# Kernel optimization log

Measured on AMD Instinct MI355X. Metric: run time of the kernel, lower is better.

Reference implementation:

```python
import jax, jax.numpy as jnp
import numpy as np

EPS = 1e-6
NH = 8     # num_head
WIN = 7    # window

def _ln(x, w, b):
    # channels_last LayerNorm over the final dim
    m = x.mean(-1, keepdims=True)
    v = ((x - m) ** 2).mean(-1, keepdims=True)
    return (x - m) / jnp.sqrt(v + EPS) * w + b

def _dwconv7(x, w, b):
    # x: (B, C, H, W); w: (C, 1, 7, 7) depthwise kernel; padding 3 (SAME for k=7)
    y = jax.lax.conv_general_dilated(
        x, w, window_strides=(1, 1), padding=((3, 3), (3, 3)),
        feature_group_count=x.shape[1],
        dimension_numbers=('NCHW', 'OIHW', 'NCHW'))
    return y + b[None, :, None, None]

def _forward(x, x_e, ln_w, ln_b, lne_w, lne_b, q_w, q_b, qcut_w, qcut_b,
             a_w, a_b, l_w, l_b, conv_w, conv_b, econv_w, econv_b,
             efore_w, efore_b, eback_w, eback_b, kv_w, kv_b,
             scl_w, scl_b, proj_w, proj_b, proje_w, proje_b):
    B, H, W, C = x.shape
    hd = C // NH // 2  # attention head dim (kv is split into k and v halves)

    xn = _ln(x, ln_w, ln_b)          # (B,H,W,C)
    xen = _ln(x_e, lne_w, lne_b)     # (B,H,W,C//2)

    # global shortcut branch (window != 0)
    short = jnp.concatenate([xn, xen], axis=3).transpose(0, 3, 1, 2)  # (B, 3C/2, H, W)

    q = xn @ q_w + q_b                # (B,H,W,C)
    cut = xn @ qcut_w + qcut_b        # (B,H,W,C//2)

    xl = jax.nn.gelu(xn @ l_w + l_b, approximate=False).transpose(0, 3, 1, 2)  # (B,C,H,W)
    a = _dwconv7(xl, conv_w, conv_b).transpose(0, 2, 3, 1) @ a_w + a_b          # (B,H,W,C)

    # kv from the activated l-branch (pre-conv)
    bfeat = xl.transpose(0, 2, 3, 1)                                  # (B,H,W,C)
    kv = (bfeat @ kv_w + kv_b).reshape(B, H * W, 2, NH, hd).transpose(2, 0, 3, 1, 4)
    k, v = kv[0], kv[1]                                               # (B,NH,HW,hd)

    # AdaptiveAvgPool2d((7,7)); H,W divisible by 7 -> exact uniform block mean
    pooled = short.reshape(B, -1, WIN, H // WIN, WIN, W // WIN).mean(axis=(3, 5))  # (B,3C/2,7,7)
    pooled = pooled.transpose(0, 2, 3, 1) @ scl_w + scl_b             # (B,7,7,C//2)
    m = pooled.reshape(B, WIN * WIN, NH, hd).transpose(0, 2, 1, 3)    # (B,NH,49,hd)

    attn = jax.nn.softmax((m * hd ** -0.5) @ jnp.swapaxes(k, -2, -1), axis=-1)  # (B,NH,49,HW)
    ao = (attn @ v).reshape(B, NH, WIN, WIN, hd).transpose(0, 1, 4, 2, 3).reshape(B, C // 2, WIN, WIN)
    ao = jax.image.resize(ao, (B, C // 2, H, W), method='bilinear').transpose(0, 2, 3, 1)  # (B,H,W,C//2)

    # depth branch: linear -> depthwise conv -> linear
    xe2 = (xen @ efore_w + efore_b).transpose(0, 3, 1, 2)             # (B,C//2,H,W)
    xe2 = _dwconv7(xe2, econv_w, econv_b).transpose(0, 2, 3, 1) @ eback_w + eback_b

    cut = cut * xe2
    xg = q * a
    cat = jnp.concatenate([xg, ao, cut], axis=3)                      # (B,H,W,2C)
    x_e_out = cat @ proje_w + proje_b                                 # (B,H,W,C//2)
    x_out = cat @ proj_w + proj_b                                     # (B,H,W,C)
    return x_out, x_e_out

def setup_inputs() -> dict:
    B, H, W, C = 16, 56, 84, 256
    key = jax.random.key(0)
    ks = jax.random.split(key, 16)
    def lin(k, din, dout):
        return jax.random.normal(k, (din, dout), jnp.float32) * float(1.0 / np.sqrt(din))
    return {
        'x': jax.random.normal(ks[0], (B, H, W, C), jnp.float32),
        'x_e': jax.random.normal(ks[1], (B, H, W, C // 2), jnp.float32),
        'ln_w': jnp.ones((C,), jnp.float32), 'ln_b': jnp.zeros((C,), jnp.float32),
        'lne_w': jnp.ones((C // 2,), jnp.float32), 'lne_b': jnp.zeros((C // 2,), jnp.float32),
        'q_w': lin(ks[2], C, C), 'q_b': jnp.zeros((C,), jnp.float32),
        'qcut_w': lin(ks[3], C, C // 2), 'qcut_b': jnp.zeros((C // 2,), jnp.float32),
        'a_w': lin(ks[4], C, C), 'a_b': jnp.zeros((C,), jnp.float32),
        'l_w': lin(ks[5], C, C), 'l_b': jnp.zeros((C,), jnp.float32),
        'conv_w': jax.random.normal(ks[6], (C, 1, 7, 7), jnp.float32) * 0.05,
        'conv_b': jnp.zeros((C,), jnp.float32),
        'econv_w': jax.random.normal(ks[7], (C // 2, 1, 7, 7), jnp.float32) * 0.05,
        'econv_b': jnp.zeros((C // 2,), jnp.float32),
        'efore_w': lin(ks[8], C // 2, C // 2), 'efore_b': jnp.zeros((C // 2,), jnp.float32),
        'eback_w': lin(ks[9], C // 2, C // 2), 'eback_b': jnp.zeros((C // 2,), jnp.float32),
        'kv_w': lin(ks[10], C, C), 'kv_b': jnp.zeros((C,), jnp.float32),
        'scl_w': lin(ks[11], C // 2 * 3, C // 2), 'scl_b': jnp.zeros((C // 2,), jnp.float32),
        'proj_w': lin(ks[12], 2 * C, C), 'proj_b': jnp.zeros((C,), jnp.float32),
        'proje_w': lin(ks[13], 2 * C, C // 2), 'proje_b': jnp.zeros((C // 2,), jnp.float32),
    }

def reference(x, x_e, ln_w, ln_b, lne_w, lne_b, q_w, q_b, qcut_w, qcut_b,
              a_w, a_b, l_w, l_b, conv_w, conv_b, econv_w, econv_b,
              efore_w, efore_b, eback_w, eback_b, kv_w, kv_b,
              scl_w, scl_b, proj_w, proj_b, proje_w, proje_b):
    return _forward(x, x_e, ln_w, ln_b, lne_w, lne_b, q_w, q_b, qcut_w, qcut_b,
                    a_w, a_b, l_w, l_b, conv_w, conv_b, econv_w, econv_b,
                    efore_w, efore_b, eback_w, eback_b, kv_w, kv_b,
                    scl_w, scl_b, proj_w, proj_b, proje_w, proje_b)
```

## Files before the change

### kernel.cpp

```cpp
#include <hip/hip_runtime.h>
#include <math.h>

#define N_TOK 75264
#define BDIM 16
#define HDIM 56
#define WDIM 84
#define CDIM 256
#define NHEAD 8
#define HWTOK 4704
#define NQ 49
#define SPLIT 8
#define TOKSPL 588
#define TSUB 84

typedef unsigned short u16;
typedef __attribute__((ext_vector_type(8))) short short8;
typedef __attribute__((ext_vector_type(8))) unsigned short ushort8;
typedef __attribute__((ext_vector_type(4))) float floatx4;

__device__ __forceinline__ float bf2f(u16 u) {
    return __builtin_bit_cast(float, (unsigned)u << 16);
}
__device__ __forceinline__ u16 f2bf(float f) {
    unsigned u = __builtin_bit_cast(unsigned, f);
    u += 0x7fffu + ((u >> 16) & 1u);
    return (u16)(u >> 16);
}
__device__ __forceinline__ float gelu_exact(float v) {
    return 0.5f * v * (1.0f + erff(v * 0.70710678118654752f));
}

__global__ __launch_bounds__(256)
void wsplit_kernel(const float* __restrict__ q, const float* __restrict__ qcut,
                   const float* __restrict__ a, const float* __restrict__ l,
                   const float* __restrict__ kv, const float* __restrict__ efo,
                   const float* __restrict__ eba, const float* __restrict__ proj,
                   const float* __restrict__ proje,
                   u16* __restrict__ dh, u16* __restrict__ dl)
{
    int e = blockIdx.x * 256 + threadIdx.x;
    const float* src; int N, base, le;
    if (e < 65536)       { src = q;     N = 256; base = 0;      le = e; }
    else if (e < 98304)  { src = qcut;  N = 128; base = 65536;  le = e - 65536; }
    else if (e < 163840) { src = a;     N = 256; base = 98304;  le = e - 98304; }
    else if (e < 229376) { src = l;     N = 256; base = 163840; le = e - 163840; }
    else if (e < 294912) { src = kv;    N = 256; base = 229376; le = e - 229376; }
    else if (e < 311296) { src = efo;   N = 128; base = 294912; le = e - 294912; }
    else if (e < 327680) { src = eba;   N = 128; base = 311296; le = e - 311296; }
    else if (e < 458752) { src = proj;  N = 256; base = 327680; le = e - 327680; }
    else                 { src = proje; N = 128; base = 458752; le = e - 458752; }
    int K = (base >= 327680) ? 512 : ((base >= 294912) ? 128 : 256);
    int k = le / N, n = le & (N - 1);
    float w = src[le];
    u16 h = f2bf(w);
    dh[base + n * K + k] = h;
    dl[base + n * K + k] = f2bf(w - bf2f(h));
}

__global__ __launch_bounds__(256)
void cwt_kernel(const float* __restrict__ conv_w, const float* __restrict__ econv_w,
                float* __restrict__ wt)
{
    int i = blockIdx.x * 256 + threadIdx.x;
    if (i < 12544) {
        int c = i / 49, tap = i % 49;
        wt[tap * 256 + c] = conv_w[i];
    } else if (i < 18816) {
        int j = i - 12544;
        int c = j / 49, tap = j % 49;
        wt[12544 + tap * 128 + c] = econv_w[j];
    }
}

template<int CH>
__global__ __launch_bounds__(256)
void ln_kernel(const float* __restrict__ x, const float* __restrict__ w,
               const float* __restrict__ b, u16* __restrict__ oh, u16* __restrict__ ol)
{
    const int lane = threadIdx.x & 63;
    const int wv = threadIdx.x >> 6;
    const size_t tok = (size_t)blockIdx.x * 4 + wv;
    constexpr int V = CH / 64;
    float v[V];
    float s = 0.f, sq = 0.f;
    if constexpr (CH == 256) {
        float4 t4 = *(const float4*)(x + tok * CH + lane * 4);
        v[0] = t4.x; v[1] = t4.y; v[2] = t4.z; v[3] = t4.w;
    } else {
        float2 t2 = *(const float2*)(x + tok * CH + lane * 2);
        v[0] = t2.x; v[1] = t2.y;
    }
    #pragma unroll
    for (int i = 0; i < V; ++i) { s += v[i]; sq += v[i] * v[i]; }
    #pragma unroll
    for (int off = 32; off > 0; off >>= 1) {
        s += __shfl_xor(s, off);
        sq += __shfl_xor(sq, off);
    }
    const float mean = s * (1.0f / CH);
    const float var = sq * (1.0f / CH) - mean * mean;
    const float rstd = rsqrtf(var + 1e-6f);
    u16 hh[V], ll[V];
    #pragma unroll
    for (int i = 0; i < V; ++i) {
        float o = (v[i] - mean) * rstd * w[lane * V + i] + b[lane * V + i];
        hh[i] = f2bf(o);
        ll[i] = f2bf(o - bf2f(hh[i]));
    }
    if constexpr (CH == 256) {
        ushort4 th = {hh[0], hh[1], hh[2], hh[3]};
        ushort4 tl = {ll[0], ll[1], ll[2], ll[3]};
        *(ushort4*)(oh + tok * CH + lane * 4) = th;
        *(ushort4*)(ol + tok * CH + lane * 4) = tl;
    } else {
        ushort2 th = {hh[0], hh[1]};
        ushort2 tl = {ll[0], ll[1]};
        *(ushort2*)(oh + tok * CH + lane * 2) = th;
        *(ushort2*)(ol + tok * CH + lane * 2) = tl;
    }
}

__global__ __launch_bounds__(128)
void pool_scl_kernel(const u16* __restrict__ xnh, const u16* __restrict__ xnl,
                     const u16* __restrict__ xeh, const u16* __restrict__ xel,
                     const float* __restrict__ sclw, const float* __restrict__ sclb,
                     float* __restrict__ m)
{
    __shared__ float pooled[384];
    const int bp = blockIdx.x;
    const int b = bp / 49, p = bp % 49;
    const int py = p / 7, px = p % 7;
    const int tid = threadIdx.x;
    for (int ch = tid; ch < 384; ch += 128) {
        float acc = 0.f;
        for (int i = 0; i < 96; ++i) {
            int y = py * 8 + i / 12, x = px * 12 + i % 12;
            size_t pix = ((size_t)(b * HDIM + y) * WDIM + x);
            if (ch < 256) acc += bf2f(xnh[pix * 256 + ch]) + bf2f(xnl[pix * 256 + ch]);
            else          acc += bf2f(xeh[pix * 128 + ch - 256]) + bf2f(xel[pix * 128 + ch - 256]);
        }
        pooled[ch] = acc * (1.0f / 96.0f);
    }
    __syncthreads();
    float acc = sclb[tid];
    for (int k = 0; k < 384; ++k) acc = fmaf(pooled[k], sclw[k * 128 + tid], acc);
    m[(size_t)bp * 128 + tid] = acc;
}

#define BK 32
#define PADK 40
template<int EPI>
__global__ __launch_bounds__(256, 2)
void mgemm(const u16* __restrict__ Ah, const u16* __restrict__ Al, int lda,
           const u16* __restrict__ Bh, const u16* __restrict__ Bl, int K,
           const float* __restrict__ bias,
           u16* __restrict__ Dh, u16* __restrict__ Dl,
           float* __restrict__ Df, int ldd)
{
    __shared__ u16 AsH[128 * PADK], AsL[128 * PADK], BsH[128 * PADK], BsL[128 * PADK];
    const int t = threadIdx.x;
    const int m0 = blockIdx.x * 128, n0 = blockIdx.y * 128;
    const int sr = t >> 1;
    const int sk = (t & 1) * 16;
    const int lane = t & 63;
    const int w = t >> 6;
    const int wm = w >> 1, wn = w & 1;
    const int frow = lane & 15;
    const int fko = (lane >> 4) * 8;

    const u16* pAh = Ah + (size_t)(m0 + sr) * lda + sk;
    const u16* pAl = Al + (size_t)(m0 + sr) * lda + sk;
    const u16* pBh = Bh + (size_t)(n0 + sr) * K + sk;
    const u16* pBl = Bl + (size_t)(n0 + sr) * K + sk;

    int4 rAh0 = *(const int4*)(pAh);     int4 rAh1 = *(const int4*)(pAh + 8);
    int4 rAl0 = *(const int4*)(pAl);     int4 rAl1 = *(const int4*)(pAl + 8);
    int4 rBh0 = *(const int4*)(pBh);     int4 rBh1 = *(const int4*)(pBh + 8);
    int4 rBl0 = *(const int4*)(pBl);     int4 rBl1 = *(const int4*)(pBl + 8);

    floatx4 acc[4][4] = {};

    for (int k0 = 0; k0 < K; k0 += BK) {
        __syncthreads();
        *(int4*)&AsH[sr * PADK + sk] = rAh0;  *(int4*)&AsH[sr * PADK + sk + 8] = rAh1;
        *(int4*)&AsL[sr * PADK + sk] = rAl0;  *(int4*)&AsL[sr * PADK + sk + 8] = rAl1;
        *(int4*)&BsH[sr * PADK + sk] = rBh0;  *(int4*)&BsH[sr * PADK + sk + 8] = rBh1;
        *(int4*)&BsL[sr * PADK + sk] = rBl0;  *(int4*)&BsL[sr * PADK + sk + 8] = rBl1;
        __syncthreads();
        if (k0 + BK < K) {
            rAh0 = *(const int4*)(pAh + k0 + BK);  rAh1 = *(const int4*)(pAh + k0 + BK + 8);
            rAl0 = *(const int4*)(pAl + k0 + BK);  rAl1 = *(const int4*)(pAl + k0 + BK + 8);
            rBh0 = *(const int4*)(pBh + k0 + BK);  rBh1 = *(const int4*)(pBh + k0 + BK + 8);
            rBl0 = *(const int4*)(pBl + k0 + BK);  rBl1 = *(const int4*)(pBl + k0 + BK + 8);
        }
        short8 afh[4], afl[4], bfh[4], bfl[4];
        #pragma unroll
        for (int i = 0; i < 4; ++i) {
            int ar = wm * 64 + i * 16 + frow;
            afh[i] = *(const short8*)&AsH[ar * PADK + fko];
            afl[i] = *(const short8*)&AsL[ar * PADK + fko];
            int bc = wn * 64 + i * 16 + frow;
            bfh[i] = *(const short8*)&BsH[bc * PADK + fko];
            bfl[i] = *(const short8*)&BsL[bc * PADK + fko];
        }
        #pragma unroll
        for (int mt = 0; mt < 4; ++mt)
        #pragma unroll
        for (int nt = 0; nt < 4; ++nt) {
            acc[mt][nt] = __builtin_amdgcn_mfma_f32_16x16x32_bf16(afh[mt], bfh[nt], acc[mt][nt], 0, 0, 0);
            acc[mt][nt] = __builtin_amdgcn_mfma_f32_16x16x32_bf16(afh[mt], bfl[nt], acc[mt][nt], 0, 0, 0);
            acc[mt][nt] = __builtin_amdgcn_mfma_f32_16x16x32_bf16(afl[mt], bfh[nt], acc[mt][nt], 0, 0, 0);
        }
    }

    #pragma unroll
    for (int mt = 0; mt < 4; ++mt)
    #pragma unroll
    for (int nt = 0; nt < 4; ++nt)
    #pragma unroll
    for (int i = 0; i < 4; ++i) {
        int r = m0 + wm * 64 + mt * 16 + (lane >> 4) * 4 + i;
        int c = n0 + wn * 64 + nt * 16 + (lane & 15);
        float v = acc[mt][nt][i] + bias[c];
        size_t off = (size_t)r * ldd + c;
        if constexpr (EPI == 1) v = gelu_exact(v);
        if constexpr (EPI == 2) v *= bf2f(Dh[off]) + bf2f(Dl[off]);
        if constexpr (EPI == 3) {
            Df[off] = v;
        } else {
            u16 h = f2bf(v);
            Dh[off] = h;
            Dl[off] = f2bf(v - bf2f(h));
        }
    }
}

template<int C>
__global__ __launch_bounds__(256)
void dwconv7_kernel(const u16* __restrict__ inh, const u16* __restrict__ inl,
                    const float* __restrict__ wT, const float* __restrict__ bias,
                    u16* __restrict__ outh, u16* __restrict__ outl)
{
    constexpr int CPW = C / 8;
    const int gid = blockIdx.x * 256 + threadIdx.x;
    const int cw = gid & (CPW - 1);
    const int p = gid / CPW;
    const int c = cw * 8;
    const int x = p % WDIM;
    int tmp = p / WDIM;
    const int y = tmp % HDIM;
    const int b = tmp / HDIM;
    float acc[8];
    {
        float4 b0 = *(const float4*)(bias + c);
        float4 b1 = *(const float4*)(bias + c + 4);
        acc[0] = b0.x; acc[1] = b0.y; acc[2] = b0.z; acc[3] = b0.w;
        acc[4] = b1.x; acc[5] = b1.y; acc[6] = b1.z; acc[7] = b1.w;
    }
    for (int ky = 0; ky < 7; ++ky) {
        int yy = y + ky - 3;
        if (yy < 0 || yy >= HDIM) continue;
        const size_t rowoff = ((size_t)(b * HDIM + yy) * WDIM) * C;
        #pragma unroll
        for (int kx = 0; kx < 7; ++kx) {
            int xx = x + kx - 3;
            if (xx < 0 || xx >= WDIM) continue;
            ushort8 ih = *(const ushort8*)(inh + rowoff + (size_t)xx * C + c);
            ushort8 il = *(const ushort8*)(inl + rowoff + (size_t)xx * C + c);
            const float* wp = wT + (ky * 7 + kx) * C + c;
            float4 w0 = *(const float4*)(wp);
            float4 w1 = *(const float4*)(wp + 4);
            acc[0] = fmaf(bf2f(ih[0]) + bf2f(il[0]), w0.x, acc[0]);
            acc[1] = fmaf(bf2f(ih[1]) + bf2f(il[1]), w0.y, acc[1]);
            acc[2] = fmaf(bf2f(ih[2]) + bf2f(il[2]), w0.z, acc[2]);
            acc[3] = fmaf(bf2f(ih[3]) + bf2f(il[3]), w0.w, acc[3]);
            acc[4] = fmaf(bf2f(ih[4]) + bf2f(il[4]), w1.x, acc[4]);
            acc[5] = fmaf(bf2f(ih[5]) + bf2f(il[5]), w1.y, acc[5]);
            acc[6] = fmaf(bf2f(ih[6]) + bf2f(il[6]), w1.z, acc[6]);
            acc[7] = fmaf(bf2f(ih[7]) + bf2f(il[7]), w1.w, acc[7]);
        }
    }
    ushort8 oh, ol;
    #pragma unroll
    for (int j = 0; j < 8; ++j) {
        u16 h = f2bf(acc[j]);
        oh[j] = h;
        ol[j] = f2bf(acc[j] - bf2f(h));
    }
    *(ushort8*)(outh + (size_t)p * C + c) = oh;
    *(ushort8*)(outl + (size_t)p * C + c) = ol;
}

__global__ __launch_bounds__(256)
void attn_part_kernel(const float* __restrict__ m, const u16* __restrict__ kvh,
                      const u16* __restrict__ kvl,
                      float* __restrict__ Opart, float* __restrict__ mpart,
                      float* __restrict__ lpart)
{
    __shared__ float mq[NQ * 17];
    __shared__ float Ks[TSUB * 16];
    __shared__ float Vs[TSUB * 16];
    __shared__ float St[NQ * 85];
    __shared__ float Osm[NQ * 16];
    __shared__ float rowm[NQ], rowl[NQ], rowscale[NQ], rownewm[NQ];
    const int blk = blockIdx.x;
    const int bh = blk >> 3, s = blk & 7;
    const int b = bh >> 3, h = bh & 7;
    const int tid = threadIdx.x;
    const int tbase = s * TOKSPL;
    for (int i = tid; i < NQ * 16; i += 256) {
        int p = i >> 4, d = i & 15;
        mq[p * 17 + d] = m[((size_t)(b * 49 + p)) * 128 + h * 16 + d] * 0.25f;
        Osm[i] = 0.f;
    }
    if (tid < NQ) { rowm[tid] = -3.4e38f; rowl[tid] = 0.f; }
    __syncthreads();
    for (int c0 = 0; c0 < TOKSPL; c0 += TSUB) {
        const int t0 = tbase + c0;
        for (int i = tid; i < TSUB * 4; i += 256) {
            int row = i >> 2, q = (i & 3) << 2;
            size_t base = ((size_t)(b * HWTOK + t0 + row)) * 256 + h * 16 + q;
            ushort4 kh = *(const ushort4*)(kvh + base);
            ushort4 kl = *(const ushort4*)(kvl + base);
            ushort4 vh = *(const ushort4*)(kvh + base + 128);
            ushort4 vl = *(const ushort4*)(kvl + base + 128);
            Ks[row * 16 + q + 0] = bf2f(kh.x) + bf2f(kl.x);
            Ks[row * 16 + q + 1] = bf2f(kh.y) + bf2f(kl.y);
            Ks[row * 16 + q + 2] = bf2f(kh.z) + bf2f(kl.z);
            Ks[row * 16 + q + 3] = bf2f(kh.w) + bf2f(kl.w);
            Vs[row * 16 + q + 0] = bf2f(vh.x) + bf2f(vl.x);
            Vs[row * 16 + q + 1] = bf2f(vh.y) + bf2f(vl.y);
            Vs[row * 16 + q + 2] = bf2f(vh.z) + bf2f(vl.z);
            Vs[row * 16 + q + 3] = bf2f(vh.w) + bf2f(vl.w);
        }
        __syncthreads();
        for (int i = tid; i < NQ * TSUB; i += 256) {
            int p = i % NQ, t = i / NQ;
            const float* mp = &mq[p * 17];
            const float* kp = &Ks[t * 16];
            float sv = 0.f;
            #pragma unroll
            for (int d = 0; d < 16; ++d) sv = fmaf(mp[d], kp[d], sv);
            St[p * 85 + t] = sv;
        }
        __syncthreads();
        if (tid < NQ) {
            float mx = -3.4e38f;
            const float* sr = &St[tid * 85];
            for (int t = 0; t < TSUB; ++t) mx = fmaxf(mx, sr[t]);
            float nm = fmaxf(rowm[tid], mx);
            rownewm[tid] = nm;
            rowscale[tid] = expf(rowm[tid] - nm);
        }
        __syncthreads();
        for (int i = tid; i < NQ * TSUB; i += 256) {
            int p = i / TSUB, t = i % TSUB;
            St[p * 85 + t] = expf(St[p * 85 + t] - rownewm[p]);
        }
        __syncthreads();
        if (tid < NQ) {
            float sv = 0.f;
            const float* sr = &St[tid * 85];
            for (int t = 0; t < TSUB; ++t) sv += sr[t];
            rowl[tid] = rowl[tid] * rowscale[tid] + sv;
            rowm[tid] = rownewm[tid];
        }
        for (int i = tid; i < NQ * 16; i += 256) {
            int p = i >> 4, d = i & 15;
            float acc = Osm[i] * rowscale[p];
            const float* sr = &St[p * 85];
            const float* vp = &Vs[d];
            #pragma unroll 6
            for (int t = 0; t < TSUB; ++t) acc = fmaf(sr[t], vp[t * 16], acc);
            Osm[i] = acc;
        }
        __syncthreads();
    }
    for (int i = tid; i < NQ * 16; i += 256)
        Opart[(size_t)blk * (NQ * 16) + i] = Osm[i];
    if (tid < NQ) {
        mpart[blk * NQ + tid] = rowm[tid];
        lpart[blk * NQ + tid] = rowl[tid];
    }
}

__global__ __launch_bounds__(256)
void attn_combine_kernel(const float* __restrict__ Opart, const float* __restrict__ mpart,
                         const float* __restrict__ lpart, float* __restrict__ ao)
{
    const int bh = blockIdx.x;
    const int b = bh >> 3, h = bh & 7;
    const int tid = threadIdx.x;
    for (int i = tid; i < NQ * 16; i += 256) {
        int p = i >> 4, d = i & 15;
        float M = -3.4e38f;
        #pragma unroll
        for (int s = 0; s < SPLIT; ++s)
            M = fmaxf(M, mpart[(bh * SPLIT + s) * NQ + p]);
        float sO = 0.f, sl = 0.f;
        #pragma unroll
        for (int s = 0; s < SPLIT; ++s) {
            float e = expf(mpart[(bh * SPLIT + s) * NQ + p] - M);
            sl = fmaf(lpart[(bh * SPLIT + s) * NQ + p], e, sl);
            sO = fmaf(Opart[(size_t)(bh * SPLIT + s) * (NQ * 16) + i], e, sO);
        }
        ao[((size_t)(b * 49 + p)) * 128 + h * 16 + d] = sO / sl;
    }
}

__global__ __launch_bounds__(256)
void resize_kernel(const float* __restrict__ ao, u16* __restrict__ cath,
                   u16* __restrict__ catl)
{
    const int idx = blockIdx.x * 256 + threadIdx.x;
    const int c = idx & 127;
    const int p = idx >> 7;
    const int x = p % WDIM;
    int tmp = p / WDIM;
    const int y = tmp % HDIM;
    const int b = tmp / HDIM;
    float fy = (y + 0.5f) * 0.125f - 0.5f;
    float fx = (x + 0.5f) * (1.0f / 12.0f) - 0.5f;
    float yf = floorf(fy), xf = floorf(fx);
    int y0 = (int)yf, x0 = (int)xf;
    float wy = fy - yf, wx = fx - xf;
    int y1 = y0 + 1 < 6 ? y0 + 1 : 6;
    int x1 = x0 + 1 < 6 ? x0 + 1 : 6;
    y0 = y0 > 0 ? y0 : 0;
    x0 = x0 > 0 ? x0 : 0;
    const float* base = ao + (size_t)b * 49 * 128 + c;
    float v00 = base[(y0 * 7 + x0) * 128], v01 = base[(y0 * 7 + x1) * 128];
    float v10 = base[(y1 * 7 + x0) * 128], v11 = base[(y1 * 7 + x1) * 128];
    float r = (1.f - wy) * ((1.f - wx) * v00 + wx * v01)
            + wy * ((1.f - wx) * v10 + wx * v11);
    u16 h = f2bf(r);
    cath[(size_t)p * 512 + 256 + c] = h;
    catl[(size_t)p * 512 + 256 + c] = f2bf(r - bf2f(h));
}

extern "C" void kernel_launch(void* const* d_in, const int* in_sizes, int n_in,
                              void* d_out, int out_size, void* d_ws, size_t ws_size,
                              hipStream_t stream) {
    const float* x       = (const float*)d_in[0];
    const float* x_e     = (const float*)d_in[1];
    const float* ln_w    = (const float*)d_in[2];
    const float* ln_b    = (const float*)d_in[3];
    const float* lne_w   = (const float*)d_in[4];
    const float* lne_b   = (const float*)d_in[5];
    const float* q_w     = (const float*)d_in[6];
    const float* q_b     = (const float*)d_in[7];
    const float* qcut_w  = (const float*)d_in[8];
    const float* qcut_b  = (const float*)d_in[9];
    const float* a_w     = (const float*)d_in[10];
    const float* a_b     = (const float*)d_in[11];
    const float* l_w     = (const float*)d_in[12];
    const float* l_b     = (const float*)d_in[13];
    const float* conv_w  = (const float*)d_in[14];
    const float* conv_b  = (const float*)d_in[15];
    const float* econv_w = (const float*)d_in[16];
    const float* econv_b = (const float*)d_in[17];
    const float* efore_w = (const float*)d_in[18];
    const float* efore_b = (const float*)d_in[19];
    const float* eback_w = (const float*)d_in[20];
    const float* eback_b = (const float*)d_in[21];
    const float* kv_w    = (const float*)d_in[22];
    const float* kv_b    = (const float*)d_in[23];
    const float* scl_w   = (const float*)d_in[24];
    const float* scl_b   = (const float*)d_in[25];
    const float* proj_w  = (const float*)d_in[26];
    const float* proj_b  = (const float*)d_in[27];
    const float* proje_w = (const float*)d_in[28];
    const float* proje_b = (const float*)d_in[29];

    float* out_x = (float*)d_out;
    float* out_e = out_x + (size_t)N_TOK * 256;

    const size_t NT = N_TOK;

    u16* doutU = (u16*)d_out;
    u16* xlH  = doutU;
    u16* xlL  = xlH  + NT * 256;
    u16* xenH = xlL  + NT * 256;
    u16* xenL = xenH + NT * 128;

    u16* ws   = (u16*)d_ws;
    u16* xnH  = ws;
    u16* xnL  = xnH  + NT * 256;
    u16* catH = xnL  + NT * 256;
    u16* catL = catH + NT * 512;
    u16* wtH  = catL + NT * 512;
    u16* wtL  = wtH  + 524288;
    float* mbuf  = (float*)(wtL + 524288);
    float* aosm  = mbuf + 16 * 49 * 128;
    float* Opart = aosm + 16 * 49 * 128;
    float* mpart = Opart + 1024 * NQ * 16;
    float* lpart = mpart + 1024 * NQ;
    float* cwT   = lpart + 1024 * NQ;
    float* ecwT  = cwT + 12544;

    u16 *qtH = wtH + 0,      *qtL = wtL + 0;
    u16 *qctH = wtH + 65536, *qctL = wtL + 65536;
    u16 *atH = wtH + 98304,  *atL = wtL + 98304;
    u16 *ltH = wtH + 163840, *ltL = wtL + 163840;
    u16 *kvtH = wtH + 229376,*kvtL = wtL + 229376;
    u16 *efH = wtH + 294912, *efL = wtL + 294912;
    u16 *ebH = wtH + 311296, *ebL = wtL + 311296;
    u16 *pjH = wtH + 327680, *pjL = wtL + 327680;
    u16 *peH = wtH + 458752, *peL = wtL + 458752;

    u16 *cvH = xnH, *cvL = xnL;
    u16 *kvH = xnH, *kvL = xnL;
    u16 *e1H = xlH, *e1L = xlH + NT * 128;
    u16 *e2H = xlL, *e2L = xlL + NT * 128;

    dim3 g2(588, 2), g1(588, 1);

    wsplit_kernel<<<2048, 256, 0, stream>>>(q_w, qcut_w, a_w, l_w, kv_w, efore_w,
                                            eback_w, proj_w, proje_w, wtH, wtL);
    cwt_kernel<<<74, 256, 0, stream>>>(conv_w, econv_w, cwT);

    ln_kernel<256><<<N_TOK / 4, 256, 0, stream>>>(x, ln_w, ln_b, xnH, xnL);
    ln_kernel<128><<<N_TOK / 4, 256, 0, stream>>>(x_e, lne_w, lne_b, xenH, xenL);
    pool_scl_kernel<<<16 * 49, 128, 0, stream>>>(xnH, xnL, xenH, xenL, scl_w, scl_b, mbuf);

    mgemm<0><<<g2, 256, 0, stream>>>(xnH, xnL, 256, qtH, qtL, 256, q_b,
                                     catH, catL, nullptr, 512);
    mgemm<0><<<g1, 256, 0, stream>>>(xnH, xnL, 256, qctH, qctL, 256, qcut_b,
                                     catH + 384, catL + 384, nullptr, 512);
    mgemm<1><<<g2, 256, 0, stream>>>(xnH, xnL, 256, ltH, ltL, 256, l_b,
                                     xlH, xlL, nullptr, 256);
    dwconv7_kernel<256><<<(N_TOK * 32) / 256, 256, 0, stream>>>(xlH, xlL, cwT, conv_b, cvH, cvL);
    mgemm<2><<<g2, 256, 0, stream>>>(cvH, cvL, 256, atH, atL, 256, a_b,
                                     catH, catL, nullptr, 512);
    mgemm<0><<<g2, 256, 0, stream>>>(xlH, xlL, 256, kvtH, kvtL, 256, kv_b,
                                     kvH, kvL, nullptr, 256);
    attn_part_kernel<<<BDIM * NHEAD * SPLIT, 256, 0, stream>>>(mbuf, kvH, kvL,
                                                               Opart, mpart, lpart);
    attn_combine_kernel<<<BDIM * NHEAD, 256, 0, stream>>>(Opart, mpart, lpart, aosm);
    resize_kernel<<<(N_TOK * 128) / 256, 256, 0, stream>>>(aosm, catH, catL);

    mgemm<0><<<g1, 256, 0, stream>>>(xenH, xenL, 128, efH, efL, 128, efore_b,
                                     e1H, e1L, nullptr, 128);
    dwconv7_kernel<128><<<(N_TOK * 16) / 256, 256, 0, stream>>>(e1H, e1L, ecwT, econv_b, e2H, e2L);
    mgemm<2><<<g1, 256, 0, stream>>>(e2H, e2L, 128, ebH, ebL, 128, eback_b,
                                     catH + 384, catL + 384, nullptr, 512);
    mgemm<3><<<g2, 256, 0, stream>>>(catH, catL, 512, pjH, pjL, 512, proj_b,
                                     nullptr, nullptr, out_x, 256);
    mgemm<3><<<g1, 256, 0, stream>>>(catH, catL, 512, peH, peL, 512, proje_b,
                                     nullptr, nullptr, out_e, 128);
}
```

Baseline: 1.358 ms.

## Store conv inputs as fp32 and compute four output rows per dwconv thread

The l-branch GELU output and the efore output are now written as fp32 instead of bf16 hi/lo pairs. The kv GEMM gains an A-source mode that reads fp32 and splits it into hi/lo in registers. The depthwise 7x7 conv now computes four vertically adjacent output pixels per thread, so each loaded input row feeds up to four accumulators, and it reads one fp32 buffer instead of two bf16 planes. This is meant to cut global loads in the conv and drop the per-element hi/lo recombination, at the cost of more registers per conv thread and an extra conversion in the kv GEMM load path.

```diff
diff --git a/kernel.cpp b/kernel.cpp
--- a/kernel.cpp
+++ b/kernel.cpp
@@ -149,9 +149,10 @@
 
 #define BK 32
 #define PADK 40
-template<int EPI>
+template<int EPI, int ASRC>
 __global__ __launch_bounds__(256, 2)
-void mgemm(const u16* __restrict__ Ah, const u16* __restrict__ Al, int lda,
+void mgemm(const u16* __restrict__ Ah, const u16* __restrict__ Al,
+           const float* __restrict__ Af, int lda,
            const u16* __restrict__ Bh, const u16* __restrict__ Bl, int K,
            const float* __restrict__ bias,
            u16* __restrict__ Dh, u16* __restrict__ Dl,
@@ -168,30 +169,63 @@
     const int frow = lane & 15;
     const int fko = (lane >> 4) * 8;
 
-    const u16* pAh = Ah + (size_t)(m0 + sr) * lda + sk;
-    const u16* pAl = Al + (size_t)(m0 + sr) * lda + sk;
     const u16* pBh = Bh + (size_t)(n0 + sr) * K + sk;
     const u16* pBl = Bl + (size_t)(n0 + sr) * K + sk;
-
-    int4 rAh0 = *(const int4*)(pAh);     int4 rAh1 = *(const int4*)(pAh + 8);
-    int4 rAl0 = *(const int4*)(pAl);     int4 rAl1 = *(const int4*)(pAl + 8);
     int4 rBh0 = *(const int4*)(pBh);     int4 rBh1 = *(const int4*)(pBh + 8);
     int4 rBl0 = *(const int4*)(pBl);     int4 rBl1 = *(const int4*)(pBl + 8);
 
+    const u16* pAh = nullptr; const u16* pAl = nullptr; const float* pAf = nullptr;
+    int4 rAh0, rAh1, rAl0, rAl1;
+    float4 rf0, rf1, rf2, rf3;
+    if constexpr (ASRC == 0) {
+        pAh = Ah + (size_t)(m0 + sr) * lda + sk;
+        pAl = Al + (size_t)(m0 + sr) * lda + sk;
+        rAh0 = *(const int4*)(pAh);  rAh1 = *(const int4*)(pAh + 8);
+        rAl0 = *(const int4*)(pAl);  rAl1 = *(const int4*)(pAl + 8);
+    } else {
+        pAf = Af + (size_t)(m0 + sr) * lda + sk;
+        rf0 = *(const float4*)(pAf);      rf1 = *(const float4*)(pAf + 4);
+        rf2 = *(const float4*)(pAf + 8);  rf3 = *(const float4*)(pAf + 12);
+    }
+
     floatx4 acc[4][4] = {};
 
     for (int k0 = 0; k0 < K; k0 += BK) {
         __syncthreads();
-        *(int4*)&AsH[sr * PADK + sk] = rAh0;  *(int4*)&AsH[sr * PADK + sk + 8] = rAh1;
-        *(int4*)&AsL[sr * PADK + sk] = rAl0;  *(int4*)&AsL[sr * PADK + sk + 8] = rAl1;
+        if constexpr (ASRC == 0) {
+            *(int4*)&AsH[sr * PADK + sk] = rAh0;  *(int4*)&AsH[sr * PADK + sk + 8] = rAh1;
+            *(int4*)&AsL[sr * PADK + sk] = rAl0;  *(int4*)&AsL[sr * PADK + sk + 8] = rAl1;
+        } else {
+            float fv[16] = {rf0.x, rf0.y, rf0.z, rf0.w, rf1.x, rf1.y, rf1.z, rf1.w,
+                            rf2.x, rf2.y, rf2.z, rf2.w, rf3.x, rf3.y, rf3.z, rf3.w};
+            ushort8 h0, h1, l0, l1;
+            #pragma unroll
+            for (int j = 0; j < 8; ++j) {
+                unsigned ua = __builtin_bit_cast(unsigned, fv[j]);
+                u16 ha = (u16)(ua >> 16);
+                h0[j] = ha;
+                l0[j] = f2bf(fv[j] - bf2f(ha));
+                unsigned ub = __builtin_bit_cast(unsigned, fv[j + 8]);
+                u16 hb = (u16)(ub >> 16);
+                h1[j] = hb;
+                l1[j] = f2bf(fv[j + 8] - bf2f(hb));
+            }
+            *(ushort8*)&AsH[sr * PADK + sk] = h0;  *(ushort8*)&AsH[sr * PADK + sk + 8] = h1;
+            *(ushort8*)&AsL[sr * PADK + sk] = l0;  *(ushort8*)&AsL[sr * PADK + sk + 8] = l1;
+        }
         *(int4*)&BsH[sr * PADK + sk] = rBh0;  *(int4*)&BsH[sr * PADK + sk + 8] = rBh1;
         *(int4*)&BsL[sr * PADK + sk] = rBl0;  *(int4*)&BsL[sr * PADK + sk + 8] = rBl1;
         __syncthreads();
         if (k0 + BK < K) {
-            rAh0 = *(const int4*)(pAh + k0 + BK);  rAh1 = *(const int4*)(pAh + k0 + BK + 8);
-            rAl0 = *(const int4*)(pAl + k0 + BK);  rAl1 = *(const int4*)(pAl + k0 + BK + 8);
-            rBh0 = *(const int4*)(pBh + k0 + BK);  rBh1 = *(const int4*)(pBh + k0 + BK + 8);
-            rBl0 = *(const int4*)(pBl + k0 + BK);  rBl1 = *(const int4*)(pBl + k0 + BK + 8);
+            if constexpr (ASRC == 0) {
+                rAh0 = *(const int4*)(pAh + k0 + BK);  rAh1 = *(const int4*)(pAh + k0 + BK + 8);
+                rAl0 = *(const int4*)(pAl + k0 + BK);  rAl1 = *(const int4*)(pAl + k0 + BK + 8);
+            } else {
+                rf0 = *(const float4*)(pAf + k0 + BK);      rf1 = *(const float4*)(pAf + k0 + BK + 4);
+                rf2 = *(const float4*)(pAf + k0 + BK + 8);  rf3 = *(const float4*)(pAf + k0 + BK + 12);
+            }
+            rBh0 = *(const int4*)(pBh + (size_t)(k0 + BK));  rBh1 = *(const int4*)(pBh + (size_t)(k0 + BK) + 8);
+            rBl0 = *(const int4*)(pBl + (size_t)(k0 + BK));  rBl1 = *(const int4*)(pBl + (size_t)(k0 + BK) + 8);
         }
         short8 afh[4], afl[4], bfh[4], bfl[4];
         #pragma unroll
@@ -223,11 +257,12 @@
         int c = n0 + wn * 64 + nt * 16 + (lane & 15);
         float v = acc[mt][nt][i] + bias[c];
         size_t off = (size_t)r * ldd + c;
-        if constexpr (EPI == 1) v = gelu_exact(v);
-        if constexpr (EPI == 2) v *= bf2f(Dh[off]) + bf2f(Dl[off]);
-        if constexpr (EPI == 3) {
+        if constexpr (EPI == 1) {
+            Df[off] = gelu_exact(v);
+        } else if constexpr (EPI == 3) {
             Df[off] = v;
         } else {
+            if constexpr (EPI == 2) v *= bf2f(Dh[off]) + bf2f(Dl[off]);
             u16 h = f2bf(v);
             Dh[off] = h;
             Dl[off] = f2bf(v - bf2f(h));
@@ -237,58 +272,68 @@
 
 template<int C>
 __global__ __launch_bounds__(256)
-void dwconv7_kernel(const u16* __restrict__ inh, const u16* __restrict__ inl,
-                    const float* __restrict__ wT, const float* __restrict__ bias,
+void dwconv7_kernel(const float* __restrict__ in, const float* __restrict__ wT,
+                    const float* __restrict__ bias,
                     u16* __restrict__ outh, u16* __restrict__ outl)
 {
     constexpr int CPW = C / 8;
     const int gid = blockIdx.x * 256 + threadIdx.x;
-    const int cw = gid & (CPW - 1);
-    const int p = gid / CPW;
+    const int cw = gid % CPW;
     const int c = cw * 8;
-    const int x = p % WDIM;
-    int tmp = p / WDIM;
-    const int y = tmp % HDIM;
-    const int b = tmp / HDIM;
-    float acc[8];
+    int t2 = gid / CPW;
+    const int x = t2 % WDIM;
+    int t3 = t2 / WDIM;
+    const int ys = t3 % (HDIM / 4);
+    const int b = t3 / (HDIM / 4);
+    const int y0 = ys * 4;
+    float acc[4][8];
     {
         float4 b0 = *(const float4*)(bias + c);
         float4 b1 = *(const float4*)(bias + c + 4);
-        acc[0] = b0.x; acc[1] = b0.y; acc[2] = b0.z; acc[3] = b0.w;
-        acc[4] = b1.x; acc[5] = b1.y; acc[6] = b1.z; acc[7] = b1.w;
-    }
-    for (int ky = 0; ky < 7; ++ky) {
-        int yy = y + ky - 3;
+        #pragma unroll
+        for (int s = 0; s < 4; ++s) {
+            acc[s][0] = b0.x; acc[s][1] = b0.y; acc[s][2] = b0.z; acc[s][3] = b0.w;
+            acc[s][4] = b1.x; acc[s][5] = b1.y; acc[s][6] = b1.z; acc[s][7] = b1.w;
+        }
+    }
+    #pragma unroll
+    for (int r = 0; r < 10; ++r) {
+        int yy = y0 + r - 3;
         if (yy < 0 || yy >= HDIM) continue;
-        const size_t rowoff = ((size_t)(b * HDIM + yy) * WDIM) * C;
         #pragma unroll
         for (int kx = 0; kx < 7; ++kx) {
             int xx = x + kx - 3;
             if (xx < 0 || xx >= WDIM) continue;
-            ushort8 ih = *(const ushort8*)(inh + rowoff + (size_t)xx * C + c);
-            ushort8 il = *(const ushort8*)(inl + rowoff + (size_t)xx * C + c);
-            const float* wp = wT + (ky * 7 + kx) * C + c;
-            float4 w0 = *(const float4*)(wp);
-            float4 w1 = *(const float4*)(wp + 4);
-            acc[0] = fmaf(bf2f(ih[0]) + bf2f(il[0]), w0.x, acc[0]);
-            acc[1] = fmaf(bf2f(ih[1]) + bf2f(il[1]), w0.y, acc[1]);
-            acc[2] = fmaf(bf2f(ih[2]) + bf2f(il[2]), w0.z, acc[2]);
-            acc[3] = fmaf(bf2f(ih[3]) + bf2f(il[3]), w0.w, acc[3]);
-            acc[4] = fmaf(bf2f(ih[4]) + bf2f(il[4]), w1.x, acc[4]);
-            acc[5] = fmaf(bf2f(ih[5]) + bf2f(il[5]), w1.y, acc[5]);
-            acc[6] = fmaf(bf2f(ih[6]) + bf2f(il[6]), w1.z, acc[6]);
-            acc[7] = fmaf(bf2f(ih[7]) + bf2f(il[7]), w1.w, acc[7]);
-        }
-    }
-    ushort8 oh, ol;
-    #pragma unroll
-    for (int j = 0; j < 8; ++j) {
-        u16 h = f2bf(acc[j]);
-        oh[j] = h;
-        ol[j] = f2bf(acc[j] - bf2f(h));
-    }
-    *(ushort8*)(outh + (size_t)p * C + c) = oh;
-    *(ushort8*)(outl + (size_t)p * C + c) = ol;
+            const float* ip = in + ((size_t)((b * HDIM + yy) * WDIM + xx)) * C + c;
+            float4 i0 = *(const float4*)ip;
+            float4 i1 = *(const float4*)(ip + 4);
+            float iv[8] = {i0.x, i0.y, i0.z, i0.w, i1.x, i1.y, i1.z, i1.w};
+            #pragma unroll
+            for (int s = 0; s < 4; ++s) {
+                if (r - s < 0 || r - s > 6) continue;
+                const float* wp = wT + ((r - s) * 7 + kx) * C + c;
+                float4 w0 = *(const float4*)wp;
+                float4 w1 = *(const float4*)(wp + 4);
+                float wv[8] = {w0.x, w0.y, w0.z, w0.w, w1.x, w1.y, w1.z, w1.w};
+                #pragma unroll
+                for (int j = 0; j < 8; ++j)
+                    acc[s][j] = fmaf(iv[j], wv[j], acc[s][j]);
+            }
+        }
+    }
+    #pragma unroll
+    for (int s = 0; s < 4; ++s) {
+        size_t pix = (size_t)((b * HDIM + y0 + s) * WDIM + x);
+        ushort8 oh, ol;
+        #pragma unroll
+        for (int j = 0; j < 8; ++j) {
+            u16 h = f2bf(acc[s][j]);
+            oh[j] = h;
+            ol[j] = f2bf(acc[s][j] - bf2f(h));
+        }
+        *(ushort8*)(outh + pix * C + c) = oh;
+        *(ushort8*)(outl + pix * C + c) = ol;
+    }
 }
 
 __global__ __launch_bounds__(256)
@@ -477,11 +522,12 @@
 
     const size_t NT = N_TOK;
 
-    u16* doutU = (u16*)d_out;
-    u16* xlH  = doutU;
-    u16* xlL  = xlH  + NT * 256;
-    u16* xenH = xlL  + NT * 256;
-    u16* xenL = xenH + NT * 128;
+    float* xlF  = (float*)d_out;
+    float* e1F  = xlF;
+    u16*   e2H  = (u16*)(xlF + NT * 128);
+    u16*   e2L  = e2H + NT * 128;
+    u16*   xenH = (u16*)(xlF + NT * 256);
+    u16*   xenL = xenH + NT * 128;
 
     u16* ws   = (u16*)d_ws;
     u16* xnH  = ws;
@@ -510,8 +556,6 @@
 
     u16 *cvH = xnH, *cvL = xnL;
     u16 *kvH = xnH, *kvL = xnL;
-    u16 *e1H = xlH, *e1L = xlH + NT * 128;
-    u16 *e2H = xlL, *e2L = xlL + NT * 128;
 
     dim3 g2(588, 2), g1(588, 1);
 
@@ -523,29 +567,29 @@
     ln_kernel<128><<<N_TOK / 4, 256, 0, stream>>>(x_e, lne_w, lne_b, xenH, xenL);
     pool_scl_kernel<<<16 * 49, 128, 0, stream>>>(xnH, xnL, xenH, xenL, scl_w, scl_b, mbuf);
 
-    mgemm<0><<<g2, 256, 0, stream>>>(xnH, xnL, 256, qtH, qtL, 256, q_b,
-                                     catH, catL, nullptr, 512);
-    mgemm<0><<<g1, 256, 0, stream>>>(xnH, xnL, 256, qctH, qctL, 256, qcut_b,
-                                     catH + 384, catL + 384, nullptr, 512);
-    mgemm<1><<<g2, 256, 0, stream>>>(xnH, xnL, 256, ltH, ltL, 256, l_b,
-                                     xlH, xlL, nullptr, 256);
-    dwconv7_kernel<256><<<(N_TOK * 32) / 256, 256, 0, stream>>>(xlH, xlL, cwT, conv_b, cvH, cvL);
-    mgemm<2><<<g2, 256, 0, stream>>>(cvH, cvL, 256, atH, atL, 256, a_b,
-                                     catH, catL, nullptr, 512);
-    mgemm<0><<<g2, 256, 0, stream>>>(xlH, xlL, 256, kvtH, kvtL, 256, kv_b,
-                                     kvH, kvL, nullptr, 256);
+    mgemm<0, 0><<<g2, 256, 0, stream>>>(xnH, xnL, nullptr, 256, qtH, qtL, 256, q_b,
+                                        catH, catL, nullptr, 512);
+    mgemm<0, 0><<<g1, 256, 0, stream>>>(xnH, xnL, nullptr, 256, qctH, qctL, 256, qcut_b,
+                                        catH + 384, catL + 384, nullptr, 512);
+    mgemm<1, 0><<<g2, 256, 0, stream>>>(xnH, xnL, nullptr, 256, ltH, ltL, 256, l_b,
+                                        nullptr, nullptr, xlF, 256);
+    dwconv7_kernel<256><<<(N_TOK / 4) * 32 / 256, 256, 0, stream>>>(xlF, cwT, conv_b, cvH, cvL);
+    mgemm<2, 0><<<g2, 256, 0, stream>>>(cvH, cvL, nullptr, 256, atH, atL, 256, a_b,
+                                        catH, catL, nullptr, 512);
+    mgemm<0, 1><<<g2, 256, 0, stream>>>(nullptr, nullptr, xlF, 256, kvtH, kvtL, 256, kv_b,
+                                        kvH, kvL, nullptr, 256);
     attn_part_kernel<<<BDIM * NHEAD * SPLIT, 256, 0, stream>>>(mbuf, kvH, kvL,
                                                                Opart, mpart, lpart);
     attn_combine_kernel<<<BDIM * NHEAD, 256, 0, stream>>>(Opart, mpart, lpart, aosm);
     resize_kernel<<<(N_TOK * 128) / 256, 256, 0, stream>>>(aosm, catH, catL);
 
-    mgemm<0><<<g1, 256, 0, stream>>>(xenH, xenL, 128, efH, efL, 128, efore_b,
-                                     e1H, e1L, nullptr, 128);
-    dwconv7_kernel<128><<<(N_TOK * 16) / 256, 256, 0, stream>>>(e1H, e1L, ecwT, econv_b, e2H, e2L);
-    mgemm<2><<<g1, 256, 0, stream>>>(e2H, e2L, 128, ebH, ebL, 128, eback_b,
-                                     catH + 384, catL + 384, nullptr, 512);
-    mgemm<3><<<g2, 256, 0, stream>>>(catH, catL, 512, pjH, pjL, 512, proj_b,
-                                     nullptr, nullptr, out_x, 256);
-    mgemm<3><<<g1, 256, 0, stream>>>(catH, catL, 512, peH, peL, 512, proje_b,
-                                     nullptr, nullptr, out_e, 128);
-}
+    mgemm<3, 0><<<g1, 256, 0, stream>>>(xenH, xenL, nullptr, 128, efH, efL, 128, efore_b,
+                                        nullptr, nullptr, e1F, 128);
+    dwconv7_kernel<128><<<(N_TOK / 4) * 16 / 256, 256, 0, stream>>>(e1F, ecwT, econv_b, e2H, e2L);
+    mgemm<2, 0><<<g1, 256, 0, stream>>>(e2H, e2L, nullptr, 128, ebH, ebL, 128, eback_b,
+                                        catH + 384, catL + 384, nullptr, 512);
+    mgemm<3, 0><<<g2, 256, 0, stream>>>(catH, catL, nullptr, 512, pjH, pjL, 512, proj_b,
+                                        nullptr, nullptr, out_x, 256);
+    mgemm<3, 0><<<g1, 256, 0, stream>>>(catH, catL, nullptr, 512, peH, peL, 512, proje_b,
+                                        nullptr, nullptr, out_e, 128);
+}
```

Measured after the change: 1.351 ms. About the same (-0.5%).
